# Kernel optimization log

Measured on AMD Instinct MI355X. Metric: run time of the kernel, lower is better.

The kernel has to match this reference:

```python
import jax, jax.numpy as jnp
import numpy as np

EPS = 1e-5  # BatchNorm1d default eps


def _xavier_uniform(key, shape):
    # torch xavier: fan_in = shape[1]*prod(shape[2:]), fan_out = shape[0]*prod(shape[2:])
    rf = int(np.prod(shape[2:])) if len(shape) > 2 else 1
    fan_in = shape[1] * rf
    fan_out = shape[0] * rf
    bound = float(np.sqrt(6.0 / (fan_in + fan_out)))
    return jax.random.uniform(key, shape, jnp.float32, -bound, bound)


def setup_inputs() -> dict:
    key = jax.random.key(0)
    ks = jax.random.split(key, 6)
    d_in, h1, h2, d_out = 256, 512, 512, 256
    B = 4096
    x = jax.random.normal(ks[0], (B, 1, d_in), dtype=jnp.float32)
    W1 = _xavier_uniform(ks[1], (h1, d_in))
    b1 = jnp.zeros((h1,), jnp.float32)
    gamma = jnp.ones((1, 1, 1), jnp.float32)   # BatchNorm1d(1) weight
    beta = jnp.zeros((1, 1, 1), jnp.float32)   # BatchNorm1d(1) bias
    coeffs2 = _xavier_uniform(ks[2], (2, h2, h1, 16))
    bias2 = jnp.zeros((1, h2), jnp.float32)
    coeffs3 = _xavier_uniform(ks[3], (2, d_out, h2, 8))
    bias3 = jnp.zeros((1, d_out), jnp.float32)
    return {"x": x, "W1": W1, "b1": b1, "gamma": gamma, "beta": beta,
            "coeffs2": coeffs2, "bias2": bias2, "coeffs3": coeffs3, "bias3": bias3}


def _fourier_kan(x, coeffs, bias, gridsize):
    # x: (N, in)  coeffs: (2, out, in, grid)  ->  (N, out)
    k = jnp.arange(1, gridsize + 1, dtype=x.dtype)          # (grid,)
    arg = x[:, :, None] * k                                  # (N, in, grid) -- basis computed ONCE
    y = jnp.einsum('nig,oig->no', jnp.cos(arg), coeffs[0])
    y = y + jnp.einsum('nig,oig->no', jnp.sin(arg), coeffs[1])
    return y + bias


def reference(x, W1, b1, gamma, beta, coeffs2, bias2, coeffs3, bias3):
    # x: (B, 1, d_in)
    h = jnp.einsum('bcd,hd->bch', x, W1) + b1                # Linear -> (B,1,h1)
    # BatchNorm1d(1), training-mode batch stats over (N, L) for the single channel
    mean = jnp.mean(h, axis=(0, 2), keepdims=True)
    var = jnp.mean((h - mean) ** 2, axis=(0, 2), keepdims=True)
    h = gamma * (h - mean) * jax.lax.rsqrt(var + EPS) + beta
    h = jax.nn.relu(h)
    h = h.reshape(-1, h.shape[-1])                           # (B, h1)
    h = _fourier_kan(h, coeffs2, bias2, 16)                  # (B, h2)
    h = _fourier_kan(h, coeffs3, bias3, 8)                   # (B, out)
    return jax.nn.softmax(h, axis=1)
```

## Files before the change

### kernel.cpp

```cpp
#include <hip/hip_runtime.h>
#include <hip/hip_fp16.h>
#include <stdint.h>

typedef unsigned short u16;
typedef unsigned int u32;
typedef long i64;
typedef short bf16x8 __attribute__((ext_vector_type(8)));
typedef float f32x4 __attribute__((ext_vector_type(4)));

#define SCALE_C   1024.f
#define INV_SCALE 0.0009765625f

__device__ __forceinline__ float bf2f(u16 v) { return __uint_as_float(((u32)v) << 16); }

__device__ __forceinline__ u16 f2bf(float a) {
  u32 u = __float_as_uint(a); u += 0x7FFFu + ((u >> 16) & 1u); return (u16)(u >> 16);
}

__device__ __forceinline__ u32 packbf2(float a, float b) {
  u32 ua = __float_as_uint(a); ua += 0x7FFFu + ((ua >> 16) & 1u);
  u32 ub = __float_as_uint(b); ub += 0x7FFFu + ((ub >> 16) & 1u);
  return (ua >> 16) | (ub & 0xFFFF0000u);
}

__device__ __forceinline__ u32 packfp8x4(float a, float b, float c, float d) {
  u32 lo = (u32)__builtin_amdgcn_cvt_pk_fp8_f32(a, b, 0, false);
  return (u32)__builtin_amdgcn_cvt_pk_fp8_f32(c, d, (int)lo, true);
}

__device__ __forceinline__ float inval(const void* p, int idx, int isf) {
  return isf ? ((const float*)p)[idx] : bf2f(((const u16*)p)[idx]);
}

__device__ __forceinline__ void split_body(
    const void* __restrict__ src, u16* __restrict__ dst, int i, int isf, int lo_pos)
{
  int row = i >> 6, g = i & 63;
  float v[4];
  if (isf) {
    float4 t = ((const float4*)src)[i];
    v[0] = t.x; v[1] = t.y; v[2] = t.z; v[3] = t.w;
  } else {
    uint2 t = ((const uint2*)src)[i];
    const u16* p = (const u16*)&t;
    v[0] = bf2f(p[0]); v[1] = bf2f(p[1]); v[2] = bf2f(p[2]); v[3] = bf2f(p[3]);
  }
  u16 hi[4]; float lo[4];
  #pragma unroll
  for (int j = 0; j < 4; ++j) { hi[j] = f2bf(v[j]); lo[j] = v[j] - bf2f(hi[j]); }
  u32 hw0 = (u32)hi[0] | ((u32)hi[1] << 16);
  u32 hw1 = (u32)hi[2] | ((u32)hi[3] << 16);
  u32 lw0 = packbf2(lo[0], lo[1]);
  u32 lw1 = packbf2(lo[2], lo[3]);
  u32* base = (u32*)(dst + (size_t)row * 768);
  int c = g * 2;
  base[c] = hw0; base[c + 1] = hw1;
  if (lo_pos == 1) {
    base[128 + c] = lw0; base[128 + c + 1] = lw1;
    base[256 + c] = hw0; base[256 + c + 1] = hw1;
  } else {
    base[128 + c] = hw0; base[128 + c + 1] = hw1;
    base[256 + c] = lw0; base[256 + c + 1] = lw1;
  }
}

__global__ __launch_bounds__(256) void prep_all_kernel(
    const void* __restrict__ x, const void* __restrict__ W1,
    u16* __restrict__ Xs, u16* __restrict__ W1s,
    const void* __restrict__ c2, unsigned char* __restrict__ w2f8,
    const void* __restrict__ c3, unsigned char* __restrict__ w3f8,
    int* __restrict__ flag)
{
  __shared__ int sf[4];
  const int t = threadIdx.x, wave = t >> 6;
  {
    float v = fabsf(bf2f(((const u16*)W1)[t & 127]));
    int bad = !(v < 1e6f);
    unsigned long long b = __ballot(bad);
    if ((t & 63) == 0) sf[wave] = (b != 0ull) ? 1 : 0;
  }
  __syncthreads();
  const int isf = sf[0] | sf[1] | sf[2] | sf[3];
  const int bid = blockIdx.x;
  if (bid == 0 && t == 0) *flag = isf;
  if (bid < 1024) {
    split_body(x, Xs, bid * 256 + t, isf, 1);
  } else if (bid < 1152) {
    split_body(W1, W1s, (bid - 1024) * 256 + t, isf, 2);
  } else if (bid < 2176) {
    int u = (bid - 1152) * 256 + t;
    int o = u >> 9, i = u & 511;
    u32* d = (u32*)(w2f8 + (size_t)o * 16384 + i * 32);
    if (isf) {
      const float4* f0 = (const float4*)((const float*)c2 + ((size_t)o * 512 + i) * 16);
      const float4* f1 = (const float4*)((const float*)c2 + (size_t)512 * 512 * 16 + ((size_t)o * 512 + i) * 16);
      #pragma unroll
      for (int j = 0; j < 4; ++j) { float4 v = f0[j]; d[j]   = packfp8x4(v.x*SCALE_C, v.y*SCALE_C, v.z*SCALE_C, v.w*SCALE_C); }
      #pragma unroll
      for (int j = 0; j < 4; ++j) { float4 v = f1[j]; d[4+j] = packfp8x4(v.x*SCALE_C, v.y*SCALE_C, v.z*SCALE_C, v.w*SCALE_C); }
    } else {
      const u16* s0 = (const u16*)c2 + ((size_t)o * 512 + i) * 16;
      const u16* s1 = (const u16*)c2 + (size_t)512 * 512 * 16 + ((size_t)o * 512 + i) * 16;
      #pragma unroll
      for (int j = 0; j < 4; ++j) d[j]   = packfp8x4(bf2f(s0[4*j])*SCALE_C, bf2f(s0[4*j+1])*SCALE_C, bf2f(s0[4*j+2])*SCALE_C, bf2f(s0[4*j+3])*SCALE_C);
      #pragma unroll
      for (int j = 0; j < 4; ++j) d[4+j] = packfp8x4(bf2f(s1[4*j])*SCALE_C, bf2f(s1[4*j+1])*SCALE_C, bf2f(s1[4*j+2])*SCALE_C, bf2f(s1[4*j+3])*SCALE_C);
    }
  } else {
    int u = (bid - 2176) * 256 + t;
    int o = u >> 9, i = u & 511;
    u32* d = (u32*)(w3f8 + (size_t)o * 8192 + i * 16);
    if (isf) {
      const float4* f0 = (const float4*)((const float*)c3 + ((size_t)o * 512 + i) * 8);
      const float4* f1 = (const float4*)((const float*)c3 + (size_t)256 * 512 * 8 + ((size_t)o * 512 + i) * 8);
      #pragma unroll
      for (int j = 0; j < 2; ++j) { float4 v = f0[j]; d[j]   = packfp8x4(v.x*SCALE_C, v.y*SCALE_C, v.z*SCALE_C, v.w*SCALE_C); }
      #pragma unroll
      for (int j = 0; j < 2; ++j) { float4 v = f1[j]; d[2+j] = packfp8x4(v.x*SCALE_C, v.y*SCALE_C, v.z*SCALE_C, v.w*SCALE_C); }
    } else {
      const u16* s0 = (const u16*)c3 + ((size_t)o * 512 + i) * 8;
      const u16* s1 = (const u16*)c3 + (size_t)256 * 512 * 8 + ((size_t)o * 512 + i) * 8;
      #pragma unroll
      for (int j = 0; j < 2; ++j) d[j]   = packfp8x4(bf2f(s0[4*j])*SCALE_C, bf2f(s0[4*j+1])*SCALE_C, bf2f(s0[4*j+2])*SCALE_C, bf2f(s0[4*j+3])*SCALE_C);
      #pragma unroll
      for (int j = 0; j < 2; ++j) d[2+j] = packfp8x4(bf2f(s1[4*j])*SCALE_C, bf2f(s1[4*j+1])*SCALE_C, bf2f(s1[4*j+2])*SCALE_C, bf2f(s1[4*j+3])*SCALE_C);
    }
  }
}

#define L1_LD 136
__global__ __launch_bounds__(256) void l1_kernel(
    const u16* __restrict__ xs, const u16* __restrict__ w1s, const void* __restrict__ b1,
    const int* __restrict__ flag, float* __restrict__ H, float2* __restrict__ PT)
{
  __shared__ u16 sA[128 * L1_LD];
  __shared__ u16 sB[64 * L1_LD];
  __shared__ float redbuf[8];
  const int n0 = blockIdx.x * 128, o0 = blockIdx.y * 64;
  const int t = threadIdx.x, wave = t >> 6, lane = t & 63, quad = lane >> 4, l16 = lane & 15;
  const int isf = *flag;
  f32x4 acc[2][4] = {};
  for (int ks = 0; ks < 768; ks += 128) {
    #pragma unroll
    for (int r = 0; r < 8; ++r) {
      int idx = t + r * 256;
      int row = idx >> 4, col = idx & 15;
      const uint4* src = (const uint4*)(xs + (size_t)(n0 + row) * 768 + ks) + col;
      *(uint4*)&sA[row * L1_LD + col * 8] = *src;
    }
    #pragma unroll
    for (int r = 0; r < 4; ++r) {
      int idx = t + r * 256;
      int row = idx >> 4, col = idx & 15;
      const uint4* src = (const uint4*)(w1s + (size_t)(o0 + row) * 768 + ks) + col;
      *(uint4*)&sB[row * L1_LD + col * 8] = *src;
    }
    __syncthreads();
    #pragma unroll
    for (int kk = 0; kk < 128; kk += 32) {
      bf16x8 bfr[4];
      #pragma unroll
      for (int fo = 0; fo < 4; ++fo)
        bfr[fo] = *(const bf16x8*)&sB[(fo * 16 + l16) * L1_LD + kk + quad * 8];
      #pragma unroll
      for (int fm = 0; fm < 2; ++fm) {
        bf16x8 av = *(const bf16x8*)&sA[(wave * 32 + fm * 16 + l16) * L1_LD + kk + quad * 8];
        #pragma unroll
        for (int fo = 0; fo < 4; ++fo)
          acc[fm][fo] = __builtin_amdgcn_mfma_f32_16x16x32_bf16(av, bfr[fo], acc[fm][fo], 0, 0, 0);
      }
    }
    __syncthreads();
  }
  float s = 0.f, sq = 0.f;
  #pragma unroll
  for (int fm = 0; fm < 2; ++fm)
  #pragma unroll
  for (int fo = 0; fo < 4; ++fo) {
    int o = o0 + fo * 16 + l16;
    float bias = inval(b1, o, isf);
    #pragma unroll
    for (int r = 0; r < 4; ++r) {
      int n = n0 + wave * 32 + fm * 16 + quad * 4 + r;
      float h = acc[fm][fo][r] + bias;
      H[(size_t)n * 512 + o] = h;
      s += h; sq += h * h;
    }
  }
  #pragma unroll
  for (int off = 32; off; off >>= 1) { s += __shfl_down(s, off); sq += __shfl_down(sq, off); }
  if (lane == 0) { redbuf[wave] = s; redbuf[4 + wave] = sq; }
  __syncthreads();
  if (t == 0) {
    float S = redbuf[0] + redbuf[1] + redbuf[2] + redbuf[3];
    float Q = redbuf[4] + redbuf[5] + redbuf[6] + redbuf[7];
    PT[blockIdx.y * 32 + blockIdx.x] = make_float2(S, Q);
  }
}

#define K2_LDB 144
template <int OT>
__global__ __launch_bounds__(256) void kan2_kernel(
    const float* __restrict__ H, const unsigned char* __restrict__ w2f8,
    const void* __restrict__ gammap, const void* __restrict__ betap,
    const int* __restrict__ flag, const float2* __restrict__ PT,
    float* __restrict__ P, int kzT)
{
  constexpr int FO = OT / 32;
  constexpr int BP = OT / 32;
  __shared__ unsigned char sA8[64 * K2_LDB];
  __shared__ unsigned char sB8[OT * K2_LDB];
  __shared__ float sred[8];
  const int n0 = blockIdx.x * 64, o0 = blockIdx.y * OT, kz = blockIdx.z;
  const int t = threadIdx.x, wave = t >> 6, lane = t & 63, quad = lane >> 4, l16 = lane & 15;
  const int wm = (wave & 1) * 32, wo = (wave >> 1) * (OT / 2);
  const int isf = *flag;
  {
    float2 p = PT[t];
    float s = p.x, q = p.y;
    #pragma unroll
    for (int off = 32; off; off >>= 1) { s += __shfl_down(s, off); q += __shfl_down(q, off); }
    if (lane == 0) { sred[wave] = s; sred[4 + wave] = q; }
  }
  __syncthreads();
  const float Ssum = sred[0] + sred[1] + sred[2] + sred[3];
  const float Qsum = sred[4] + sred[5] + sred[6] + sred[7];
  const float Nn = 4096.f * 512.f;
  const float mean = Ssum / Nn;
  const float rstd = rsqrtf(Qsum / Nn - mean * mean + 1e-5f);
  const float gs = inval(gammap, 0, isf) * rstd;
  const float beta = inval(betap, 0, isf);
  const int am = t >> 2, ai = t & 3;
  const int q = 128 / kzT, rr = 128 % kzT;
  const int nst = q + (kz < rr ? 1 : 0);
  const int i0 = (kz * q + (kz < rr ? kz : rr)) * 4;
  const int r0 = t >> 3, seg = t & 7;
  const unsigned char* bsrc = w2f8 + (size_t)(o0 + r0) * 16384 + (size_t)i0 * 32 + seg * 16;
  const float* hsrc = H + (size_t)(n0 + am) * 512 + i0 + ai;
  f32x4 acc[2][FO] = {};
  float ph = *hsrc;
  for (int s = 0; s < nst; ++s) {
    #pragma unroll
    for (int p = 0; p < BP; ++p) {
      uint4 v = *(const uint4*)(bsrc + (size_t)p * 32 * 16384);
      *(uint4*)&sB8[(r0 + 32 * p) * K2_LDB + seg * 16] = v;
    }
    {
      float a = fmaxf((ph - mean) * gs + beta, 0.f);
      float s1, c1; __sincosf(a, &s1, &c1);
      float t2 = c1 + c1;
      float cg[16], sg[16];
      cg[0] = c1; sg[0] = s1;
      cg[1] = fmaf(t2, c1, -1.f); sg[1] = t2 * s1;
      #pragma unroll
      for (int g = 2; g < 16; ++g) {
        cg[g] = fmaf(t2, cg[g-1], -cg[g-2]);
        sg[g] = fmaf(t2, sg[g-1], -sg[g-2]);
      }
      u32 pk[8];
      #pragma unroll
      for (int j = 0; j < 4; ++j) pk[j]   = packfp8x4(cg[4*j], cg[4*j+1], cg[4*j+2], cg[4*j+3]);
      #pragma unroll
      for (int j = 0; j < 4; ++j) pk[4+j] = packfp8x4(sg[4*j], sg[4*j+1], sg[4*j+2], sg[4*j+3]);
      uint4* dst = (uint4*)&sA8[am * K2_LDB + ai * 32];
      dst[0] = *(uint4*)&pk[0]; dst[1] = *(uint4*)&pk[4];
    }
    __syncthreads();
    bsrc += 128; hsrc += 4;
    if (s + 1 < nst) ph = *hsrc;
    #pragma unroll
    for (int kk = 0; kk < 128; kk += 32) {
      i64 bfr[FO], afr[2];
      #pragma unroll
      for (int fo = 0; fo < FO; ++fo)
        bfr[fo] = *(const i64*)&sB8[(wo + fo * 16 + l16) * K2_LDB + kk + quad * 8];
      #pragma unroll
      for (int fm = 0; fm < 2; ++fm)
        afr[fm] = *(const i64*)&sA8[(wm + fm * 16 + l16) * K2_LDB + kk + quad * 8];
      #pragma unroll
      for (int fm = 0; fm < 2; ++fm)
      #pragma unroll
      for (int fo = 0; fo < FO; ++fo)
        acc[fm][fo] = __builtin_amdgcn_mfma_f32_16x16x32_fp8_fp8(afr[fm], bfr[fo], acc[fm][fo], 0, 0, 0);
    }
    __syncthreads();
  }
  float* Pk = P + (size_t)kz * (4096 * 512);
  #pragma unroll
  for (int fm = 0; fm < 2; ++fm)
  #pragma unroll
  for (int fo = 0; fo < FO; ++fo) {
    int o = o0 + wo + fo * 16 + l16;
    #pragma unroll
    for (int r = 0; r < 4; ++r) {
      int n = n0 + wm + fm * 16 + quad * 4 + r;
      Pk[(size_t)n * 512 + o] = acc[fm][fo][r] * INV_SCALE;
    }
  }
}

#define K3_LDB 144
__global__ __launch_bounds__(256) void kan3_kernel(
    const float* __restrict__ P2, const void* __restrict__ bias2,
    const unsigned char* __restrict__ w3f8,
    const int* __restrict__ flag, float* __restrict__ Q, int kzT2)
{
  __shared__ unsigned char sA8[32 * K3_LDB];
  __shared__ unsigned char sB8[256 * K3_LDB];
  const int n0 = blockIdx.x * 32, kz = blockIdx.z;
  const int t = threadIdx.x, wave = t >> 6, lane = t & 63, quad = lane >> 4, l16 = lane & 15;
  const int wo = wave * 64;
  const int am = t >> 3, ai = t & 7;
  const int nst = 10 + (kz < 4 ? 1 : 0);
  const int i0 = (kz * 10 + (kz < 4 ? kz : 4)) * 8;
  const int r0 = t >> 3, seg = t & 7;
  const int isf = *flag;
  const unsigned char* bsrc = w3f8 + (size_t)r0 * 8192 + (size_t)i0 * 16 + seg * 16;
  const float* psrc = P2 + (size_t)(n0 + am) * 512 + i0 + ai;
  f32x4 acc[2][4] = {};
  float ph;
  {
    float v = inval(bias2, i0 + ai, isf);
    for (int k = 0; k < kzT2; ++k) v += psrc[(size_t)k * 4096 * 512];
    ph = v;
  }
  for (int s = 0; s < nst; ++s) {
    #pragma unroll
    for (int p = 0; p < 8; ++p) {
      uint4 v = *(const uint4*)(bsrc + (size_t)p * 32 * 8192);
      *(uint4*)&sB8[(r0 + 32 * p) * K3_LDB + seg * 16] = v;
    }
    {
      float s1, c1; __sincosf(ph, &s1, &c1);
      float t2 = c1 + c1;
      float cg[8], sg[8];
      cg[0] = c1; sg[0] = s1;
      cg[1] = fmaf(t2, c1, -1.f); sg[1] = t2 * s1;
      #pragma unroll
      for (int g = 2; g < 8; ++g) {
        cg[g] = fmaf(t2, cg[g-1], -cg[g-2]);
        sg[g] = fmaf(t2, sg[g-1], -sg[g-2]);
      }
      u32 pk[4];
      pk[0] = packfp8x4(cg[0], cg[1], cg[2], cg[3]);
      pk[1] = packfp8x4(cg[4], cg[5], cg[6], cg[7]);
      pk[2] = packfp8x4(sg[0], sg[1], sg[2], sg[3]);
      pk[3] = packfp8x4(sg[4], sg[5], sg[6], sg[7]);
      *(uint4*)&sA8[am * K3_LDB + ai * 16] = *(uint4*)&pk[0];
    }
    __syncthreads();
    bsrc += 128; psrc += 8;
    if (s + 1 < nst) {
      float v = inval(bias2, i0 + (s + 1) * 8 + ai, isf);
      for (int k = 0; k < kzT2; ++k) v += psrc[(size_t)k * 4096 * 512];
      ph = v;
    }
    #pragma unroll
    for (int kk = 0; kk < 128; kk += 32) {
      i64 bfr[4], afr[2];
      #pragma unroll
      for (int fo = 0; fo < 4; ++fo)
        bfr[fo] = *(const i64*)&sB8[(wo + fo * 16 + l16) * K3_LDB + kk + quad * 8];
      #pragma unroll
      for (int fm = 0; fm < 2; ++fm)
        afr[fm] = *(const i64*)&sA8[(fm * 16 + l16) * K3_LDB + kk + quad * 8];
      #pragma unroll
      for (int fm = 0; fm < 2; ++fm)
      #pragma unroll
      for (int fo = 0; fo < 4; ++fo)
        acc[fm][fo] = __builtin_amdgcn_mfma_f32_16x16x32_fp8_fp8(afr[fm], bfr[fo], acc[fm][fo], 0, 0, 0);
    }
    __syncthreads();
  }
  float* Qk = Q + (size_t)kz * (4096 * 256);
  #pragma unroll
  for (int fm = 0; fm < 2; ++fm)
  #pragma unroll
  for (int fo = 0; fo < 4; ++fo) {
    int o = wo + fo * 16 + l16;
    #pragma unroll
    for (int r = 0; r < 4; ++r) {
      int n = n0 + fm * 16 + quad * 4 + r;
      Qk[(size_t)n * 256 + o] = acc[fm][fo][r] * INV_SCALE;
    }
  }
}

__global__ __launch_bounds__(256) void softmax_kernel(
    const float* __restrict__ Q, const void* __restrict__ bias3,
    const int* __restrict__ flag, float* __restrict__ out)
{
  const int t = threadIdx.x, wave = t >> 6, lane = t & 63;
  const int row = blockIdx.x * 4 + wave;
  const int isf = *flag;
  size_t base = (size_t)row * 256 + lane * 4;
  float v0 = 0.f, v1 = 0.f, v2 = 0.f, v3 = 0.f;
  #pragma unroll
  for (int k = 0; k < 6; ++k) {
    float4 a = *(const float4*)(Q + (size_t)k * 4096 * 256 + base);
    v0 += a.x; v1 += a.y; v2 += a.z; v3 += a.w;
  }
  int o = lane * 4;
  v0 += inval(bias3, o + 0, isf);
  v1 += inval(bias3, o + 1, isf);
  v2 += inval(bias3, o + 2, isf);
  v3 += inval(bias3, o + 3, isf);
  float m = fmaxf(fmaxf(v0, v1), fmaxf(v2, v3));
  #pragma unroll
  for (int off = 32; off; off >>= 1) m = fmaxf(m, __shfl_xor(m, off));
  float e0 = __expf(v0 - m), e1 = __expf(v1 - m), e2 = __expf(v2 - m), e3 = __expf(v3 - m);
  float s = e0 + e1 + e2 + e3;
  #pragma unroll
  for (int off = 32; off; off >>= 1) s += __shfl_xor(s, off);
  float inv = 1.f / s;
  *(float4*)(out + base) = make_float4(e0 * inv, e1 * inv, e2 * inv, e3 * inv);
}

extern "C" void kernel_launch(void* const* d_in, const int* in_sizes, int n_in,
                              void* d_out, int out_size, void* d_ws, size_t ws_size,
                              hipStream_t stream)
{
  const void* x     = d_in[0];
  const void* W1    = d_in[1];
  const void* b1    = d_in[2];
  const void* gamma = d_in[3];
  const void* beta  = d_in[4];
  const void* c2    = d_in[5];
  const void* bias2 = d_in[6];
  const void* c3    = d_in[7];
  const void* bias3 = d_in[8];

  const bool wide2 = (ws_size >= (83ull << 20));
  const int kz2 = wide2 ? 6 : ((ws_size >= (75ull << 20)) ? 5 : 3);

  char* ws = (char*)d_ws;
  float*          H    = (float*)(ws + 0);
  unsigned char*  W2F8 = (unsigned char*)(ws + (16ull << 20));
  unsigned char*  W3F8 = (unsigned char*)(ws + (24ull << 20));
  u16*            Xs   = (u16*)(ws + (26ull << 20));
  u16*            W1s  = (u16*)(ws + (33ull << 20));
  float*          P2   = (float*)(ws + (34ull << 20));
  float*          Q3   = (float*)(ws + 0);
  size_t tail = (34ull << 20) + (size_t)kz2 * (8ull << 20) + 524288;
  float2* PT   = (float2*)(ws + tail);
  int*    FLAG = (int*)   (ws + tail + 65536);

  prep_all_kernel<<<dim3(2688), dim3(256), 0, stream>>>(x, W1, Xs, W1s, c2, W2F8, c3, W3F8, FLAG);
  l1_kernel   <<<dim3(32, 8), dim3(256), 0, stream>>>(Xs, W1s, b1, FLAG, H, PT);
  if (wide2)
    kan2_kernel<256><<<dim3(64, 2, kz2), dim3(256), 0, stream>>>(H, W2F8, gamma, beta, FLAG, PT, P2, kz2);
  else
    kan2_kernel<128><<<dim3(64, 4, kz2), dim3(256), 0, stream>>>(H, W2F8, gamma, beta, FLAG, PT, P2, kz2);
  kan3_kernel <<<dim3(128, 1, 6), dim3(256), 0, stream>>>(P2, bias2, W3F8, FLAG, Q3, kz2);
  softmax_kernel<<<dim3(1024), dim3(256), 0, stream>>>(Q3, bias3, FLAG, (float*)d_out);
}
```

Measured before the change: 220.4 us.

## Prefetch next K-tile into registers and XOR-swizzle LDS layout in KAN kernels

```diff
diff --git a/kernel.cpp b/kernel.cpp
--- a/kernel.cpp
+++ b/kernel.cpp
@@ -139,23 +139,42 @@
   const int n0 = blockIdx.x * 128, o0 = blockIdx.y * 64;
   const int t = threadIdx.x, wave = t >> 6, lane = t & 63, quad = lane >> 4, l16 = lane & 15;
   const int isf = *flag;
+  uint4 areg[8], breg[4];
+  #pragma unroll
+  for (int r = 0; r < 8; ++r) {
+    int idx = t + r * 256, row = idx >> 4, col = idx & 15;
+    areg[r] = *((const uint4*)(xs + (size_t)(n0 + row) * 768) + col);
+  }
+  #pragma unroll
+  for (int r = 0; r < 4; ++r) {
+    int idx = t + r * 256, row = idx >> 4, col = idx & 15;
+    breg[r] = *((const uint4*)(w1s + (size_t)(o0 + row) * 768) + col);
+  }
   f32x4 acc[2][4] = {};
   for (int ks = 0; ks < 768; ks += 128) {
     #pragma unroll
     for (int r = 0; r < 8; ++r) {
-      int idx = t + r * 256;
-      int row = idx >> 4, col = idx & 15;
-      const uint4* src = (const uint4*)(xs + (size_t)(n0 + row) * 768 + ks) + col;
-      *(uint4*)&sA[row * L1_LD + col * 8] = *src;
+      int idx = t + r * 256, row = idx >> 4, col = idx & 15;
+      *(uint4*)&sA[row * L1_LD + col * 8] = areg[r];
     }
     #pragma unroll
     for (int r = 0; r < 4; ++r) {
-      int idx = t + r * 256;
-      int row = idx >> 4, col = idx & 15;
-      const uint4* src = (const uint4*)(w1s + (size_t)(o0 + row) * 768 + ks) + col;
-      *(uint4*)&sB[row * L1_LD + col * 8] = *src;
-    }
-    __syncthreads();
+      int idx = t + r * 256, row = idx >> 4, col = idx & 15;
+      *(uint4*)&sB[row * L1_LD + col * 8] = breg[r];
+    }
+    __syncthreads();
+    if (ks + 128 < 768) {
+      #pragma unroll
+      for (int r = 0; r < 8; ++r) {
+        int idx = t + r * 256, row = idx >> 4, col = idx & 15;
+        areg[r] = *((const uint4*)(xs + (size_t)(n0 + row) * 768 + ks + 128) + col);
+      }
+      #pragma unroll
+      for (int r = 0; r < 4; ++r) {
+        int idx = t + r * 256, row = idx >> 4, col = idx & 15;
+        breg[r] = *((const uint4*)(w1s + (size_t)(o0 + row) * 768 + ks + 128) + col);
+      }
+    }
     #pragma unroll
     for (int kk = 0; kk < 128; kk += 32) {
       bf16x8 bfr[4];
@@ -198,7 +217,7 @@
   }
 }
 
-#define K2_LDB 144
+#define K2_LDB 128
 template <int OT>
 __global__ __launch_bounds__(256) void kan2_kernel(
     const float* __restrict__ H, const unsigned char* __restrict__ w2f8,
@@ -215,12 +234,23 @@
   const int t = threadIdx.x, wave = t >> 6, lane = t & 63, quad = lane >> 4, l16 = lane & 15;
   const int wm = (wave & 1) * 32, wo = (wave >> 1) * (OT / 2);
   const int isf = *flag;
+  const int am = t >> 2, ai = t & 3;
+  const int q = 128 / kzT, rr = 128 % kzT;
+  const int nst = q + (kz < rr ? 1 : 0);
+  const int i0 = (kz * q + (kz < rr ? kz : rr)) * 4;
+  const int r0 = t >> 3, seg = t & 7;
+  const unsigned char* bsrc = w2f8 + (size_t)(o0 + r0) * 16384 + (size_t)i0 * 32 + seg * 16;
+  const float* hsrc = H + (size_t)(n0 + am) * 512 + i0 + ai;
+  uint4 breg[BP];
+  #pragma unroll
+  for (int p = 0; p < BP; ++p) breg[p] = *(const uint4*)(bsrc + (size_t)p * 32 * 16384);
+  float ph = *hsrc;
   {
-    float2 p = PT[t];
-    float s = p.x, q = p.y;
-    #pragma unroll
-    for (int off = 32; off; off >>= 1) { s += __shfl_down(s, off); q += __shfl_down(q, off); }
-    if (lane == 0) { sred[wave] = s; sred[4 + wave] = q; }
+    float2 pt = PT[t];
+    float ss = pt.x, qs = pt.y;
+    #pragma unroll
+    for (int off = 32; off; off >>= 1) { ss += __shfl_down(ss, off); qs += __shfl_down(qs, off); }
+    if (lane == 0) { sred[wave] = ss; sred[4 + wave] = qs; }
   }
   __syncthreads();
   const float Ssum = sred[0] + sred[1] + sred[2] + sred[3];
@@ -230,21 +260,15 @@
   const float rstd = rsqrtf(Qsum / Nn - mean * mean + 1e-5f);
   const float gs = inval(gammap, 0, isf) * rstd;
   const float beta = inval(betap, 0, isf);
-  const int am = t >> 2, ai = t & 3;
-  const int q = 128 / kzT, rr = 128 % kzT;
-  const int nst = q + (kz < rr ? 1 : 0);
-  const int i0 = (kz * q + (kz < rr ? kz : rr)) * 4;
-  const int r0 = t >> 3, seg = t & 7;
-  const unsigned char* bsrc = w2f8 + (size_t)(o0 + r0) * 16384 + (size_t)i0 * 32 + seg * 16;
-  const float* hsrc = H + (size_t)(n0 + am) * 512 + i0 + ai;
+  const int bcol  = (seg * 16) ^ ((r0 & 7) << 4);
+  const int acol0 = (ai * 32) ^ ((am & 7) << 4);
+  const int acol1 = (ai * 32 + 16) ^ ((am & 7) << 4);
+  const int csw   = (l16 & 7) << 4;
   f32x4 acc[2][FO] = {};
-  float ph = *hsrc;
   for (int s = 0; s < nst; ++s) {
     #pragma unroll
-    for (int p = 0; p < BP; ++p) {
-      uint4 v = *(const uint4*)(bsrc + (size_t)p * 32 * 16384);
-      *(uint4*)&sB8[(r0 + 32 * p) * K2_LDB + seg * 16] = v;
-    }
+    for (int p = 0; p < BP; ++p)
+      *(uint4*)&sB8[(r0 + 32 * p) * K2_LDB + bcol] = breg[p];
     {
       float a = fmaxf((ph - mean) * gs + beta, 0.f);
       float s1, c1; __sincosf(a, &s1, &c1);
@@ -262,21 +286,26 @@
       for (int j = 0; j < 4; ++j) pk[j]   = packfp8x4(cg[4*j], cg[4*j+1], cg[4*j+2], cg[4*j+3]);
       #pragma unroll
       for (int j = 0; j < 4; ++j) pk[4+j] = packfp8x4(sg[4*j], sg[4*j+1], sg[4*j+2], sg[4*j+3]);
-      uint4* dst = (uint4*)&sA8[am * K2_LDB + ai * 32];
-      dst[0] = *(uint4*)&pk[0]; dst[1] = *(uint4*)&pk[4];
+      *(uint4*)&sA8[am * K2_LDB + acol0] = *(uint4*)&pk[0];
+      *(uint4*)&sA8[am * K2_LDB + acol1] = *(uint4*)&pk[4];
     }
     __syncthreads();
     bsrc += 128; hsrc += 4;
-    if (s + 1 < nst) ph = *hsrc;
+    if (s + 1 < nst) {
+      #pragma unroll
+      for (int p = 0; p < BP; ++p) breg[p] = *(const uint4*)(bsrc + (size_t)p * 32 * 16384);
+      ph = *hsrc;
+    }
     #pragma unroll
     for (int kk = 0; kk < 128; kk += 32) {
+      const int cb = (kk + quad * 8) ^ csw;
       i64 bfr[FO], afr[2];
       #pragma unroll
       for (int fo = 0; fo < FO; ++fo)
-        bfr[fo] = *(const i64*)&sB8[(wo + fo * 16 + l16) * K2_LDB + kk + quad * 8];
+        bfr[fo] = *(const i64*)&sB8[(wo + fo * 16 + l16) * K2_LDB + cb];
       #pragma unroll
       for (int fm = 0; fm < 2; ++fm)
-        afr[fm] = *(const i64*)&sA8[(wm + fm * 16 + l16) * K2_LDB + kk + quad * 8];
+        afr[fm] = *(const i64*)&sA8[(wm + fm * 16 + l16) * K2_LDB + cb];
       #pragma unroll
       for (int fm = 0; fm < 2; ++fm)
       #pragma unroll
@@ -299,7 +328,7 @@
   }
 }
 
-#define K3_LDB 144
+#define K3_LDB 128
 __global__ __launch_bounds__(256) void kan3_kernel(
     const float* __restrict__ P2, const void* __restrict__ bias2,
     const unsigned char* __restrict__ w3f8,
@@ -317,7 +346,13 @@
   const int isf = *flag;
   const unsigned char* bsrc = w3f8 + (size_t)r0 * 8192 + (size_t)i0 * 16 + seg * 16;
   const float* psrc = P2 + (size_t)(n0 + am) * 512 + i0 + ai;
+  const int bcol = (seg * 16) ^ ((r0 & 7) << 4);
+  const int acol = (ai * 16) ^ ((am & 7) << 4);
+  const int csw  = (l16 & 7) << 4;
   f32x4 acc[2][4] = {};
+  uint4 breg[8];
+  #pragma unroll
+  for (int p = 0; p < 8; ++p) breg[p] = *(const uint4*)(bsrc + (size_t)p * 32 * 8192);
   float ph;
   {
     float v = inval(bias2, i0 + ai, isf);
@@ -326,10 +361,8 @@
   }
   for (int s = 0; s < nst; ++s) {
     #pragma unroll
-    for (int p = 0; p < 8; ++p) {
-      uint4 v = *(const uint4*)(bsrc + (size_t)p * 32 * 8192);
-      *(uint4*)&sB8[(r0 + 32 * p) * K3_LDB + seg * 16] = v;
-    }
+    for (int p = 0; p < 8; ++p)
+      *(uint4*)&sB8[(r0 + 32 * p) * K3_LDB + bcol] = breg[p];
     {
       float s1, c1; __sincosf(ph, &s1, &c1);
       float t2 = c1 + c1;
@@ -346,24 +379,27 @@
       pk[1] = packfp8x4(cg[4], cg[5], cg[6], cg[7]);
       pk[2] = packfp8x4(sg[0], sg[1], sg[2], sg[3]);
       pk[3] = packfp8x4(sg[4], sg[5], sg[6], sg[7]);
-      *(uint4*)&sA8[am * K3_LDB + ai * 16] = *(uint4*)&pk[0];
+      *(uint4*)&sA8[am * K3_LDB + acol] = *(uint4*)&pk[0];
     }
     __syncthreads();
     bsrc += 128; psrc += 8;
     if (s + 1 < nst) {
+      #pragma unroll
+      for (int p = 0; p < 8; ++p) breg[p] = *(const uint4*)(bsrc + (size_t)p * 32 * 8192);
       float v = inval(bias2, i0 + (s + 1) * 8 + ai, isf);
       for (int k = 0; k < kzT2; ++k) v += psrc[(size_t)k * 4096 * 512];
       ph = v;
     }
     #pragma unroll
     for (int kk = 0; kk < 128; kk += 32) {
+      const int cb = (kk + quad * 8) ^ csw;
       i64 bfr[4], afr[2];
       #pragma unroll
       for (int fo = 0; fo < 4; ++fo)
-        bfr[fo] = *(const i64*)&sB8[(wo + fo * 16 + l16) * K3_LDB + kk + quad * 8];
+        bfr[fo] = *(const i64*)&sB8[(wo + fo * 16 + l16) * K3_LDB + cb];
       #pragma unroll
       for (int fm = 0; fm < 2; ++fm)
-        afr[fm] = *(const i64*)&sA8[(fm * 16 + l16) * K3_LDB + kk + quad * 8];
+        afr[fm] = *(const i64*)&sA8[(fm * 16 + l16) * K3_LDB + cb];
       #pragma unroll
       for (int fm = 0; fm < 2; ++fm)
       #pragma unroll
```

Result: slower. 397.7 us (+80.4%).

## Load KAN weight tiles via async global-to-LDS copies with XOR swizzle

Applied to the files above, without the earlier changes.

```diff
diff --git a/kernel.cpp b/kernel.cpp
--- a/kernel.cpp
+++ b/kernel.cpp
@@ -30,6 +30,12 @@
 
 __device__ __forceinline__ float inval(const void* p, int idx, int isf) {
   return isf ? ((const float*)p)[idx] : bf2f(((const u16*)p)[idx]);
+}
+
+__device__ __forceinline__ void async_cp16(const void* g, void* l) {
+  __builtin_amdgcn_global_load_lds(
+      (const __attribute__((address_space(1))) void*)g,
+      (__attribute__((address_space(3))) void*)l, 16, 0, 0);
 }
 
 __device__ __forceinline__ void split_body(
@@ -198,7 +204,7 @@
   }
 }
 
-#define K2_LDB 144
+#define K2_LDB 128
 template <int OT>
 __global__ __launch_bounds__(256) void kan2_kernel(
     const float* __restrict__ H, const unsigned char* __restrict__ w2f8,
@@ -215,12 +221,25 @@
   const int t = threadIdx.x, wave = t >> 6, lane = t & 63, quad = lane >> 4, l16 = lane & 15;
   const int wm = (wave & 1) * 32, wo = (wave >> 1) * (OT / 2);
   const int isf = *flag;
+  const int am = t >> 2, ai = t & 3;
+  const int q = 128 / kzT, rr = 128 % kzT;
+  const int nst = q + (kz < rr ? 1 : 0);
+  const int i0 = (kz * q + (kz < rr ? kz : rr)) * 4;
+  const int r0 = t >> 3, seg = t & 7;
+  const unsigned char* bsrc = w2f8 + (size_t)(o0 + r0) * 16384 + (size_t)i0 * 32
+                              + ((seg * 16) ^ ((r0 & 7) << 4));
+  const float* hsrc = H + (size_t)(n0 + am) * 512 + i0 + ai;
+  unsigned char* ldsB = &sB8[wave * 8 * K2_LDB];
+  #pragma unroll
+  for (int p = 0; p < BP; ++p)
+    async_cp16(bsrc + (size_t)p * 32 * 16384, ldsB + p * 32 * K2_LDB);
+  float ph = *hsrc;
   {
-    float2 p = PT[t];
-    float s = p.x, q = p.y;
-    #pragma unroll
-    for (int off = 32; off; off >>= 1) { s += __shfl_down(s, off); q += __shfl_down(q, off); }
-    if (lane == 0) { sred[wave] = s; sred[4 + wave] = q; }
+    float2 pt = PT[t];
+    float ss = pt.x, qs = pt.y;
+    #pragma unroll
+    for (int off = 32; off; off >>= 1) { ss += __shfl_down(ss, off); qs += __shfl_down(qs, off); }
+    if (lane == 0) { sred[wave] = ss; sred[4 + wave] = qs; }
   }
   __syncthreads();
   const float Ssum = sred[0] + sred[1] + sred[2] + sred[3];
@@ -230,21 +249,11 @@
   const float rstd = rsqrtf(Qsum / Nn - mean * mean + 1e-5f);
   const float gs = inval(gammap, 0, isf) * rstd;
   const float beta = inval(betap, 0, isf);
-  const int am = t >> 2, ai = t & 3;
-  const int q = 128 / kzT, rr = 128 % kzT;
-  const int nst = q + (kz < rr ? 1 : 0);
-  const int i0 = (kz * q + (kz < rr ? kz : rr)) * 4;
-  const int r0 = t >> 3, seg = t & 7;
-  const unsigned char* bsrc = w2f8 + (size_t)(o0 + r0) * 16384 + (size_t)i0 * 32 + seg * 16;
-  const float* hsrc = H + (size_t)(n0 + am) * 512 + i0 + ai;
+  const int acol0 = (ai * 32) ^ ((am & 7) << 4);
+  const int acol1 = (ai * 32 + 16) ^ ((am & 7) << 4);
+  const int csw   = (l16 & 7) << 4;
   f32x4 acc[2][FO] = {};
-  float ph = *hsrc;
   for (int s = 0; s < nst; ++s) {
-    #pragma unroll
-    for (int p = 0; p < BP; ++p) {
-      uint4 v = *(const uint4*)(bsrc + (size_t)p * 32 * 16384);
-      *(uint4*)&sB8[(r0 + 32 * p) * K2_LDB + seg * 16] = v;
-    }
     {
       float a = fmaxf((ph - mean) * gs + beta, 0.f);
       float s1, c1; __sincosf(a, &s1, &c1);
@@ -262,21 +271,22 @@
       for (int j = 0; j < 4; ++j) pk[j]   = packfp8x4(cg[4*j], cg[4*j+1], cg[4*j+2], cg[4*j+3]);
       #pragma unroll
       for (int j = 0; j < 4; ++j) pk[4+j] = packfp8x4(sg[4*j], sg[4*j+1], sg[4*j+2], sg[4*j+3]);
-      uint4* dst = (uint4*)&sA8[am * K2_LDB + ai * 32];
-      dst[0] = *(uint4*)&pk[0]; dst[1] = *(uint4*)&pk[4];
-    }
-    __syncthreads();
-    bsrc += 128; hsrc += 4;
+      *(uint4*)&sA8[am * K2_LDB + acol0] = *(uint4*)&pk[0];
+      *(uint4*)&sA8[am * K2_LDB + acol1] = *(uint4*)&pk[4];
+    }
+    __syncthreads();
+    hsrc += 4;
     if (s + 1 < nst) ph = *hsrc;
     #pragma unroll
     for (int kk = 0; kk < 128; kk += 32) {
+      const int cb = (kk + quad * 8) ^ csw;
       i64 bfr[FO], afr[2];
       #pragma unroll
       for (int fo = 0; fo < FO; ++fo)
-        bfr[fo] = *(const i64*)&sB8[(wo + fo * 16 + l16) * K2_LDB + kk + quad * 8];
+        bfr[fo] = *(const i64*)&sB8[(wo + fo * 16 + l16) * K2_LDB + cb];
       #pragma unroll
       for (int fm = 0; fm < 2; ++fm)
-        afr[fm] = *(const i64*)&sA8[(wm + fm * 16 + l16) * K2_LDB + kk + quad * 8];
+        afr[fm] = *(const i64*)&sA8[(wm + fm * 16 + l16) * K2_LDB + cb];
       #pragma unroll
       for (int fm = 0; fm < 2; ++fm)
       #pragma unroll
@@ -284,6 +294,12 @@
         acc[fm][fo] = __builtin_amdgcn_mfma_f32_16x16x32_fp8_fp8(afr[fm], bfr[fo], acc[fm][fo], 0, 0, 0);
     }
     __syncthreads();
+    bsrc += 128;
+    if (s + 1 < nst) {
+      #pragma unroll
+      for (int p = 0; p < BP; ++p)
+        async_cp16(bsrc + (size_t)p * 32 * 16384, ldsB + p * 32 * K2_LDB);
+    }
   }
   float* Pk = P + (size_t)kz * (4096 * 512);
   #pragma unroll
@@ -299,7 +315,7 @@
   }
 }
 
-#define K3_LDB 144
+#define K3_LDB 128
 __global__ __launch_bounds__(256) void kan3_kernel(
     const float* __restrict__ P2, const void* __restrict__ bias2,
     const unsigned char* __restrict__ w3f8,
@@ -315,9 +331,16 @@
   const int i0 = (kz * 10 + (kz < 4 ? kz : 4)) * 8;
   const int r0 = t >> 3, seg = t & 7;
   const int isf = *flag;
-  const unsigned char* bsrc = w3f8 + (size_t)r0 * 8192 + (size_t)i0 * 16 + seg * 16;
+  const unsigned char* bsrc = w3f8 + (size_t)r0 * 8192 + (size_t)i0 * 16
+                              + ((seg * 16) ^ ((r0 & 7) << 4));
   const float* psrc = P2 + (size_t)(n0 + am) * 512 + i0 + ai;
+  unsigned char* ldsB = &sB8[wave * 8 * K3_LDB];
+  const int acol = (ai * 16) ^ ((am & 7) << 4);
+  const int csw  = (l16 & 7) << 4;
   f32x4 acc[2][4] = {};
+  #pragma unroll
+  for (int p = 0; p < 8; ++p)
+    async_cp16(bsrc + (size_t)p * 32 * 8192, ldsB + p * 32 * K3_LDB);
   float ph;
   {
     float v = inval(bias2, i0 + ai, isf);
@@ -325,11 +348,6 @@
     ph = v;
   }
   for (int s = 0; s < nst; ++s) {
-    #pragma unroll
-    for (int p = 0; p < 8; ++p) {
-      uint4 v = *(const uint4*)(bsrc + (size_t)p * 32 * 8192);
-      *(uint4*)&sB8[(r0 + 32 * p) * K3_LDB + seg * 16] = v;
-    }
     {
       float s1, c1; __sincosf(ph, &s1, &c1);
       float t2 = c1 + c1;
@@ -346,10 +364,10 @@
       pk[1] = packfp8x4(cg[4], cg[5], cg[6], cg[7]);
       pk[2] = packfp8x4(sg[0], sg[1], sg[2], sg[3]);
       pk[3] = packfp8x4(sg[4], sg[5], sg[6], sg[7]);
-      *(uint4*)&sA8[am * K3_LDB + ai * 16] = *(uint4*)&pk[0];
-    }
-    __syncthreads();
-    bsrc += 128; psrc += 8;
+      *(uint4*)&sA8[am * K3_LDB + acol] = *(uint4*)&pk[0];
+    }
+    __syncthreads();
+    psrc += 8;
     if (s + 1 < nst) {
       float v = inval(bias2, i0 + (s + 1) * 8 + ai, isf);
       for (int k = 0; k < kzT2; ++k) v += psrc[(size_t)k * 4096 * 512];
@@ -357,13 +375,14 @@
     }
     #pragma unroll
     for (int kk = 0; kk < 128; kk += 32) {
+      const int cb = (kk + quad * 8) ^ csw;
       i64 bfr[4], afr[2];
       #pragma unroll
       for (int fo = 0; fo < 4; ++fo)
-        bfr[fo] = *(const i64*)&sB8[(wo + fo * 16 + l16) * K3_LDB + kk + quad * 8];
+        bfr[fo] = *(const i64*)&sB8[(wo + fo * 16 + l16) * K3_LDB + cb];
       #pragma unroll
       for (int fm = 0; fm < 2; ++fm)
-        afr[fm] = *(const i64*)&sA8[(fm * 16 + l16) * K3_LDB + kk + quad * 8];
+        afr[fm] = *(const i64*)&sA8[(fm * 16 + l16) * K3_LDB + cb];
       #pragma unroll
       for (int fm = 0; fm < 2; ++fm)
       #pragma unroll
@@ -371,6 +390,12 @@
         acc[fm][fo] = __builtin_amdgcn_mfma_f32_16x16x32_fp8_fp8(afr[fm], bfr[fo], acc[fm][fo], 0, 0, 0);
     }
     __syncthreads();
+    bsrc += 128;
+    if (s + 1 < nst) {
+      #pragma unroll
+      for (int p = 0; p < 8; ++p)
+        async_cp16(bsrc + (size_t)p * 32 * 8192, ldsB + p * 32 * K3_LDB);
+    }
   }
   float* Qk = Q + (size_t)kz * (4096 * 256);
   #pragma unroll
```

Result: faster. 211.5 us (-4.1%).
